# Optimization experiments

Hardware: AMD Instinct MI355X
Metric: run time of the kernel (lower is better)

Reference implementation:

```python
import jax, jax.numpy as jnp
import numpy as np

OBS, PRED = 8, 12
EIN, EHID, NOISE = 64, 256, 64
GEMB = 64
DHID = EHID + NOISE  # 320
G, NPER = 8, 192
B = G * NPER


def leaky(x):
    return jnp.where(x > 0, x, 0.2 * x)


def lstm_cell(x, h, c, Wih, Whh, bih, bhh):
    gates = x @ Wih.T + bih + h @ Whh.T + bhh
    i, f, g, o = jnp.split(gates, 4, axis=-1)
    c = jax.nn.sigmoid(f) * c + jax.nn.sigmoid(i) * jnp.tanh(g)
    h = jax.nn.sigmoid(o) * jnp.tanh(c)
    return h, c


def kmeans(x, k, niter=10):
    # deterministic init: first k points (torch used randperm)
    c = x[:k]
    ar = jnp.arange(k)
    for _ in range(niter):
        d2 = ((x[:, None, :] - c[None, :, :]) ** 2).sum(-1)  # [N,k]
        a = jnp.argmin(d2, axis=1)
        onehot = (a[:, None] == ar[None, :]).astype(x.dtype)  # [N,k]
        cnt = onehot.sum(0)
        mean = (onehot.T @ x) / jnp.maximum(cnt, 1.0)[:, None]
        c = jnp.where((cnt == 0)[:, None], x[:k], mean)  # reseed dead clusters
    d2 = ((x[:, None, :] - c[None, :, :]) ** 2).sum(-1)
    return jnp.argmin(d2, axis=1)


def signed_graph(node, W_ne, b_ne, W_att, b_att):
    n, D = node.shape
    emb = node @ W_ne.T + b_ne  # [n,E]
    E = emb.shape[1]
    a_other, a_self = W_att[0, :E], W_att[0, E:]
    # e[i,j] = a_other.emb[j] + a_self.emb[i] + b  (cat([other, self]) order)
    e = (emb @ a_other)[None, :] + (emb @ a_self)[:, None] + b_att[0]
    edge = jax.nn.softmax(leaky(e), axis=0)
    edge = jnp.triu(edge, 0) + jnp.triu(edge, 1).T  # symmetrize from upper tri
    d = edge.sum(1)
    L = jnp.diag(d) - edge
    dinv = 1.0 / jnp.sqrt(d)
    L_sym = dinv[:, None] * L * dinv[None, :]
    lam, H = jnp.linalg.eigh(jax.lax.stop_gradient(L_sym))  # ascending eigvals
    H = H[:, :2]  # two smallest
    Hn = H / jnp.sqrt((H ** 2).sum(1, keepdims=True))
    labels = kmeans(Hn, int(np.ceil(n / 2)))
    same = labels[:, None] == labels[None, :]
    NEG = jnp.float32(-1e8)
    pos_alpha = jax.nn.softmax(leaky(edge * jnp.where(same, 1.0, NEG)), axis=0)
    neg_alpha = jax.nn.softmax(leaky(edge * jnp.where(same, NEG, 1.0)), axis=0)
    feat = jax.nn.relu(pos_alpha[..., None] * node[None, :, :]) + \
           jax.nn.relu(neg_alpha[..., None] * node[None, :, :])  # [n,n,D]
    return feat.sum(axis=1)


def setup_inputs():
    key = jax.random.key(0)
    ks = jax.random.split(key, 22)
    p = lambda k, s: jax.random.normal(k, s, jnp.float32) * 0.1
    starts = jnp.arange(G, dtype=jnp.int32) * NPER
    return {
        "input_traj": jax.random.normal(ks[0], (OBS + PRED, B, 2), jnp.float32),
        "enc_h0": jax.random.normal(ks[1], (B, EHID), jnp.float32),
        "enc_c0": jax.random.normal(ks[2], (B, EHID), jnp.float32),
        "noise_z": jax.random.normal(ks[3], (G, NOISE), jnp.float32),
        "W_emb": p(ks[4], (EIN, 2)), "b_emb": p(ks[5], (EIN,)),
        "Wih_e": p(ks[6], (4 * EHID, EIN)), "Whh_e": p(ks[7], (4 * EHID, EHID)),
        "bih_e": p(ks[8], (4 * EHID,)), "bhh_e": p(ks[9], (4 * EHID,)),
        "Wih_d": p(ks[10], (4 * DHID, EIN)), "Whh_d": p(ks[11], (4 * DHID, DHID)),
        "bih_d": p(ks[12], (4 * DHID,)), "bhh_d": p(ks[13], (4 * DHID,)),
        "W_out": p(ks[14], (2, DHID)), "b_out": p(ks[15], (2,)),
        "W_ne": p(ks[16], (GEMB, DHID)), "b_ne": p(ks[17], (GEMB,)),
        "W_att": p(ks[18], (1, 2 * GEMB)), "b_att": p(ks[19], (1,)),
        "seq_start_end": jnp.stack([starts, starts + NPER], axis=1),
    }


def reference(input_traj, enc_h0, enc_c0, noise_z, W_emb, b_emb,
              Wih_e, Whh_e, bih_e, bhh_e, Wih_d, Whh_d, bih_d, bhh_d,
              W_out, b_out, W_ne, b_ne, W_att, b_att, seq_start_end):
    # ---- encoder ----
    x = jax.nn.relu(input_traj @ W_emb.T + b_emb)  # [T,B,EIN]
    def step(carry, xt):
        h, c = carry
        h, c = lstm_cell(xt, h, c, Wih_e, Whh_e, bih_e, bhh_e)
        return (h, c), None
    (h_enc, _), _ = jax.lax.scan(step, (enc_h0, enc_c0), x[:OBS])
    # ---- add per-scene noise (equal-sized scenes) ----
    z = jnp.repeat(noise_z, NPER, axis=0)  # [B,NOISE]
    h = jnp.concatenate([h_enc, z], axis=1)  # [B,DHID]
    c = jnp.zeros_like(h)
    traj_out = input_traj[OBS - 1]  # [B,2]
    sg = jax.vmap(lambda nd: signed_graph(nd, W_ne, b_ne, W_att, b_att))
    preds = []
    for i in range(PRED):  # eval mode: no teacher forcing
        inp = jax.nn.relu(traj_out @ W_emb.T + b_emb)
        if i % 12 == 4:
            h = sg(h.reshape(G, NPER, DHID)).reshape(B, DHID)
        h, c = lstm_cell(inp, h, c, Wih_d, Whh_d, bih_d, bhh_d)
        traj_out = h @ W_out.T + b_out
        preds.append(traj_out)
    return jnp.stack(preds)  # [PRED,B,2]
```

## Files before the change

kernel.cpp:

```cpp
#include <hip/hip_runtime.h>
#include <hip/hip_bf16.h>

typedef __hip_bfloat16 bf16;

#define NN 192
#define NG 8
#define BB 1536
#define EHID 256
#define DH 320
#define PRED 12
#define STRD 196

#define WAVE_SYNC() do { asm volatile("" ::: "memory"); __builtin_amdgcn_wave_barrier(); } while (0)

__device__ __forceinline__ float waveSum(float v){
#pragma unroll
  for (int o = 32; o > 0; o >>= 1) v += __shfl_down(v, o);
  return v;
}
__device__ __forceinline__ double waveSumD(double v){
#pragma unroll
  for (int o = 32; o > 0; o >>= 1) v += __shfl_down(v, o);
  return v;
}
__device__ __forceinline__ float waveAllSum(float v){
#pragma unroll
  for (int o = 32; o > 0; o >>= 1) v += __shfl_xor(v, o);
  return v;
}
__device__ __forceinline__ double waveAllSumD(double v){
#pragma unroll
  for (int o = 32; o > 0; o >>= 1) v += __shfl_xor(v, o);
  return v;
}

__device__ __forceinline__ double blockSumD(double v, double* red){
  int lane = threadIdx.x & 63, wid = threadIdx.x >> 6, nw = (int)blockDim.x >> 6;
  double s = waveSumD(v);
  __syncthreads();
  if (lane == 0) red[wid] = s;
  __syncthreads();
  if (wid == 0){
    double t = (lane < nw) ? red[lane] : 0.0;
    t = waveSumD(t);
    if (lane == 0) red[0] = t;
  }
  __syncthreads();
  return red[0];
}


__global__ void k_zero_int(int* __restrict__ p, int n){
  int i = blockIdx.x*blockDim.x + threadIdx.x;
  if (i < n) p[i] = 0;
}
__global__ void k_zero_f(float* __restrict__ p, int n){
  int i = blockIdx.x*blockDim.x + threadIdx.x;
  if (i < n) p[i] = 0.f;
}

__global__ void k_probe(const unsigned short* __restrict__ src, int n, int* __restrict__ cnt){
  int tid = blockIdx.x*blockDim.x + threadIdx.x;
  int stride = gridDim.x*blockDim.x;
  int bad = 0;
  for (int j = tid; j < n; j += stride){
    float v = __uint_as_float(((unsigned int)src[j]) << 16);
    if (!(fabsf(v) < 100.f)) bad++;
  }
#pragma unroll
  for (int o = 32; o > 0; o >>= 1) bad += __shfl_down(bad, o);
  if ((threadIdx.x & 63) == 0 && bad > 0) atomicAdd(cnt, bad);
}
__global__ void k_flag(const int* __restrict__ cnt, int* __restrict__ flag){
  *flag = (*cnt > 4096) ? 1 : 0;
}

struct CvtArgs {
  const void* src[20];
  float*      dst[20];
  int         n[20];
};

__global__ void k_convert(CvtArgs a, const int* __restrict__ flag){
  int id = blockIdx.y;
  int n = a.n[id];
  float* d = a.dst[id];
  int t = blockIdx.x*blockDim.x + threadIdx.x;
  int stride = gridDim.x*blockDim.x;
  if (*flag == 0){
    const bf16* s = (const bf16*)a.src[id];
    for (int j = t; j < n; j += stride) d[j] = __bfloat162float(s[j]);
  } else {
    const float* s = (const float*)a.src[id];
    for (int j = t; j < n; j += stride) d[j] = s[j];
  }
}


__global__ void k_embed(const float* __restrict__ in, const float* __restrict__ W,
                        const float* __restrict__ b, float* __restrict__ out){
  int r = blockIdx.x, e = threadIdx.x;
  float x = in[r*2], y = in[r*2+1];
  float v = W[e*2]*x + W[e*2+1]*y + b[e];
  out[r*64+e] = v > 0.f ? v : 0.f;
}

__global__ void k_concat(const float* __restrict__ henc, const float* __restrict__ z,
                         float* __restrict__ h){
  int idx = blockIdx.x*blockDim.x + threadIdx.x;
  if (idx >= BB*DH) return;
  int b = idx / DH, j = idx - b*DH;
  h[idx] = (j < EHID) ? henc[b*EHID + j] : z[(b/NN)*64 + (j - EHID)];
}

__global__ void k_copy_f(const float* __restrict__ in, float* __restrict__ dst, int n){
  int i = blockIdx.x*blockDim.x + threadIdx.x;
  if (i < n) dst[i] = in[i];
}

__global__ __launch_bounds__(256) void k_gates(
    const float* __restrict__ A1, const float* __restrict__ W1, int K1,
    const float* __restrict__ A2, const float* __restrict__ W2, int K2,
    const float* __restrict__ b1, const float* __restrict__ b2,
    float* __restrict__ C, int N){
  __shared__ __align__(16) float As[32][68];
  __shared__ __align__(16) float Ws[32][68];
  int tid = threadIdx.x;
  int tx = tid & 15, ty = tid >> 4;
  int n0 = blockIdx.x * 64, m0 = blockIdx.y * 64;
  float acc[4][4] = {};
  for (int ph = 0; ph < 2; ++ph){
    const float* A = ph ? A2 : A1;
    const float* W = ph ? W2 : W1;
    int K = ph ? K2 : K1;
    for (int k0 = 0; k0 < K; k0 += 32){
      {
        int am = tid >> 2, ak = (tid & 3) * 8;
        const float* srcA = A + (size_t)(m0+am)*K + k0 + ak;
        float4 f0 = *(const float4*)(srcA);
        float4 f1 = *(const float4*)(srcA+4);
        As[ak+0][am]=f0.x; As[ak+1][am]=f0.y; As[ak+2][am]=f0.z; As[ak+3][am]=f0.w;
        As[ak+4][am]=f1.x; As[ak+5][am]=f1.y; As[ak+6][am]=f1.z; As[ak+7][am]=f1.w;
        const float* srcW = W + (size_t)(n0+am)*K + k0 + ak;
        float4 w0 = *(const float4*)(srcW);
        float4 w1 = *(const float4*)(srcW+4);
        Ws[ak+0][am]=w0.x; Ws[ak+1][am]=w0.y; Ws[ak+2][am]=w0.z; Ws[ak+3][am]=w0.w;
        Ws[ak+4][am]=w1.x; Ws[ak+5][am]=w1.y; Ws[ak+6][am]=w1.z; Ws[ak+7][am]=w1.w;
      }
      __syncthreads();
#pragma unroll
      for (int k = 0; k < 32; ++k){
        float4 a0 = *(const float4*)&As[k][ty*4];
        float4 b0 = *(const float4*)&Ws[k][tx*4];
        float av[4] = {a0.x, a0.y, a0.z, a0.w};
        float bv[4] = {b0.x, b0.y, b0.z, b0.w};
#pragma unroll
        for (int i = 0; i < 4; ++i)
#pragma unroll
          for (int j = 0; j < 4; ++j)
            acc[i][j] += av[i]*bv[j];
      }
      __syncthreads();
    }
  }
  float bs[4];
#pragma unroll
  for (int j = 0; j < 4; ++j){
    int col = n0 + tx*4 + j;
    bs[j] = b1[col] + b2[col];
  }
#pragma unroll
  for (int i = 0; i < 4; ++i){
    int row = m0 + ty*4 + i;
    float4 v;
    v.x = acc[i][0] + bs[0]; v.y = acc[i][1] + bs[1];
    v.z = acc[i][2] + bs[2]; v.w = acc[i][3] + bs[3];
    *(float4*)&C[(size_t)row*N + n0 + tx*4] = v;
  }
}

__global__ void k_lstm(const float* __restrict__ gates, float* __restrict__ c,
                       float* __restrict__ h, int H){
  int idx = blockIdx.x*blockDim.x + threadIdx.x;
  if (idx >= BB*H) return;
  int b = idx / H, j = idx - b*H;
  const float* g = gates + (size_t)b*4*H;
  float gi = g[j], gf = g[H+j], gg = g[2*H+j], go = g[3*H+j];
  float si = 1.f/(1.f+expf(-gi));
  float sf = 1.f/(1.f+expf(-gf));
  float so = 1.f/(1.f+expf(-go));
  float cc = sf*c[idx] + si*tanhf(gg);
  c[idx] = cc;
  h[idx] = so*tanhf(cc);
}

__global__ void k_outproj(const float* __restrict__ h, const float* __restrict__ W,
                          const float* __restrict__ bo, float* __restrict__ traj,
                          void* __restrict__ outbase, int step, const int* __restrict__ flag){
  int b = blockIdx.x, lane = threadIdx.x;
  const float* hb = h + (size_t)b*DH;
  float a0 = 0.f, a1 = 0.f;
  for (int k = lane; k < DH; k += 64){
    float hv = hb[k];
    a0 += hv*W[k];
    a1 += hv*W[DH+k];
  }
  a0 = waveSum(a0); a1 = waveSum(a1);
  if (lane == 0){
    a0 += bo[0]; a1 += bo[1];
    traj[b*2] = a0; traj[b*2+1] = a1;
    size_t idx = (size_t)step*BB*2 + (size_t)b*2;
    if (*flag == 0){
      bf16* o = (bf16*)outbase;
      o[idx] = __float2bfloat16(a0); o[idx+1] = __float2bfloat16(a1);
    } else {
      float* o = (float*)outbase;
      o[idx] = a0; o[idx+1] = a1;
    }
  }
}


__global__ void k_sg_emb(const float* __restrict__ h, const float* __restrict__ Wne,
                         const float* __restrict__ bne, const float* __restrict__ Watt,
                         double* __restrict__ sself, double* __restrict__ sother){
  int node = blockIdx.x, e = threadIdx.x;
  const float* hb = h + (size_t)node*DH;
  double acc = (double)bne[e];
  for (int k = 0; k < DH; ++k) acc += (double)hb[k]*(double)Wne[e*DH+k];
  double po = acc * (double)Watt[e];
  double ps = acc * (double)Watt[64+e];
  po = waveSumD(po); ps = waveSumD(ps);
  if (e == 0){ sother[node] = po; sself[node] = ps; }
}

__global__ void k_sg_edgecol(const double* __restrict__ sself, const double* __restrict__ sother,
                             const float* __restrict__ batt, double* __restrict__ edge){
  int g = blockIdx.x, j = threadIdx.x;
  const double* ss = sself + g*NN;
  double bb = (double)batt[0];
  double sj = sother[g*NN + j];
  double m = -1e300;
  for (int i = 0; i < NN; ++i){
    double e = ss[i] + sj + bb; e = e > 0.0 ? e : 0.2*e;
    m = fmax(m, e);
  }
  double sum = 0.0;
  for (int i = 0; i < NN; ++i){
    double e = ss[i] + sj + bb; e = e > 0.0 ? e : 0.2*e;
    sum += exp(e - m);
  }
  double* E = edge + (size_t)g*NN*NN;
  for (int i = 0; i < NN; ++i){
    double e = ss[i] + sj + bb; e = e > 0.0 ? e : 0.2*e;
    E[i*NN + j] = exp(e - m)/sum;
  }
}

__global__ void k_sg_sym(const double* __restrict__ edge, double* __restrict__ esym){
  int idx = blockIdx.x*blockDim.x + threadIdx.x;
  if (idx >= NG*NN*NN) return;
  int g = idx / (NN*NN), r = idx - g*NN*NN;
  int i = r / NN, j = r - i*NN;
  const double* E = edge + (size_t)g*NN*NN;
  esym[idx] = (i <= j) ? E[i*NN + j] : E[j*NN + i];
}

__global__ void k_sg_dsum(const double* __restrict__ esym, double* __restrict__ darr){
  int i = blockIdx.x*blockDim.x + threadIdx.x;
  if (i >= NG*NN) return;
  int g = i / NN, li = i - g*NN;
  const double* E = esym + (size_t)g*NN*NN + (size_t)li*NN;
  double s = 0.0;
  for (int j = 0; j < NN; ++j) s += E[j];
  darr[i] = fmax(s, 1e-300);
}

__global__ void k_sg_lsym(const double* __restrict__ esym, const double* __restrict__ darr,
                          float* __restrict__ Afull){
  int idx = blockIdx.x*blockDim.x + threadIdx.x;
  if (idx >= NG*NN*NN) return;
  int g = idx / (NN*NN), r = idx - g*NN*NN;
  int i = r / NN, j = r - i*NN;
  double w = esym[idx];
  double lij = (i == j) ? (darr[g*NN+i] - w) : (-w);
  Afull[(size_t)g*NN*STRD + i*STRD + j] =
      (float)(lij / (sqrt(darr[g*NN+i])*sqrt(darr[g*NN+j])));
}

__global__ __launch_bounds__(256) void k_sg_eigen(const float* __restrict__ Afull,
                                                   const double* __restrict__ darr,
                                                   double* __restrict__ v1out){
  extern __shared__ unsigned char ldsraw[];
  float*  A     = (float*)ldsraw;
  double* dd    = (double*)(ldsraw + 150528);
  double* ee    = dd + NN;
  double* yv    = ee + NN;
  double* lu_d  = yv + NN;
  double* lu_du = lu_d + NN;
  double* lu_du2= lu_du + NN;
  double* redA  = lu_du2 + NN;
  double* redB  = redA + 16;
  float*  vv    = (float*)(redB + 16);
  float*  pp    = vv + NN;
  float*  uu    = pp + NN;
  int*    lu_piv= (int*)uu;
  double* lu_dl = (double*)vv;

  int g = blockIdx.x, tid = threadIdx.x;
  int lane = tid & 63, wid = tid >> 6;

  const float* src = Afull + (size_t)g*NN*STRD;
  for (int t = tid*4; t < NN*STRD; t += 1024) *(float4*)&A[t] = *(const float4*)&src[t];
  __syncthreads();

  for (int k = 0; k < NN-65; ++k){
    int m = NN-1-k;
    int i = k+1+tid;
    float x = 0.f;
    if (tid < m){
      x = A[i*STRD + k];
      vv[i] = x;
    }
    float part = (tid > 0 && tid < m) ? x*x : 0.f;
    part = waveSum(part);
    if (lane == 0) redA[wid] = (double)part;
    __syncthreads();
    double sigma = redA[0] + redA[1] + redA[2] + redA[3];
    double alpha = (double)vv[k+1];
    double beta, tau, scale;
    if (sigma <= 1e-30){ tau = 0.0; beta = alpha; scale = 0.0; }
    else {
      beta = -copysign(sqrt(alpha*alpha + sigma), alpha);
      tau = (beta - alpha)/beta;
      scale = 1.0/(alpha - beta);
    }
    float tau_f = (float)tau, scale_f = (float)scale;
    if (tid == 0){
      dd[k] = (double)A[k*STRD + k];
      ee[k] = beta;
      A[k*STRD + k] = tau_f;
    }
    if (tau != 0.0){
      float p = 0.f, u_i = 0.f;
      if (tid < m){
        const float* Ai = A + (size_t)i*STRD;
        if (tid >= 1) A[i*STRD + k] = x*scale_f;
        u_i = (tid == 0) ? 1.f : x*scale_f;
        float acc = 0.f;
        int c = k+2, c0 = (c + 3) & ~3;
        for (; c < c0; ++c) acc += Ai[c]*vv[c];
        for (; c < NN; c += 4){
          float4 a4 = *(const float4*)&Ai[c];
          float4 v4 = *(const float4*)&vv[c];
          acc += a4.x*v4.x + a4.y*v4.y + a4.z*v4.z + a4.w*v4.w;
        }
        float s = Ai[k+1] + scale_f*acc;
        p = tau_f*s;
        pp[i] = p;
      }
      float vp = u_i*p;
      vp = waveSum(vp);
      if (lane == 0) redB[wid] = (double)vp;
      __syncthreads();
      double vtp = redB[0] + redB[1] + redB[2] + redB[3];
      float Kc_f = (float)(0.5*tau*vtp);
      if (tid < m){
        float* Ai = A + (size_t)i*STRD;
        float w_i = p - Kc_f*u_i;
        {
          float wj = pp[k+1] - Kc_f;
          Ai[k+1] -= u_i*wj + w_i;
        }
        int c = k+2, c0 = (c + 3) & ~3;
        for (; c < c0; ++c){
          float uj = vv[c]*scale_f;
          float wj = pp[c] - Kc_f*uj;
          Ai[c] -= u_i*wj + w_i*uj;
        }
        for (; c < NN; c += 4){
          float4 v4 = *(const float4*)&vv[c];
          float4 p4 = *(const float4*)&pp[c];
          float4 a4 = *(const float4*)&Ai[c];
          float u0 = v4.x*scale_f, u1 = v4.y*scale_f, u2 = v4.z*scale_f, u3 = v4.w*scale_f;
          a4.x -= u_i*(p4.x - Kc_f*u0) + w_i*u0;
          a4.y -= u_i*(p4.y - Kc_f*u1) + w_i*u1;
          a4.z -= u_i*(p4.z - Kc_f*u2) + w_i*u2;
          a4.w -= u_i*(p4.w - Kc_f*u3) + w_i*u3;
          *(float4*)&Ai[c] = a4;
        }
      }
      __syncthreads();
    } else {
      __syncthreads();
    }
  }

  if (wid != 0) return;

  {
    float* uu_s = uu;
    float* ww_s = uu + 96;
    for (int k = NN-65; k < NN-2; ++k){
      int m = NN-1-k;
      int i = k+1+lane;
      bool act = lane < m;
      float x = act ? A[i*STRD + k] : 0.f;
      float part = (lane > 0) ? x*x : 0.f;
      float sig_f = waveAllSum(part);
      float alpha_f = __shfl(x, 0);
      double sigma = (double)sig_f;
      double alpha = (double)alpha_f;
      double beta, tau, scale;
      if (sigma <= 1e-30){ tau = 0.0; beta = alpha; scale = 0.0; }
      else {
        beta = -copysign(sqrt(alpha*alpha + sigma), alpha);
        tau = (beta - alpha)/beta;
        scale = 1.0/(alpha - beta);
      }
      float tau_f = (float)tau, scale_f = (float)scale;
      if (lane == 0){
        dd[k] = (double)A[k*STRD + k];
        ee[k] = beta;
        A[k*STRD + k] = tau_f;
      }
      if (tau == 0.0) continue;
      float u = (lane == 0) ? 1.f : x*scale_f;
      int base4 = (k+1) & ~3;
      int ph = (k+1) - base4;
      uu_s[lane + ph] = u;
      if (lane >= 1 && act) A[i*STRD + k] = u;
      WAVE_SYNC();
      int ic = act ? i : (k+1);
      const float* Ai = A + (size_t)ic*STRD;
      float acc = 0.f;
      {
        int c = k+1, c0 = (c + 3) & ~3;
        for (; c < c0; ++c) acc += Ai[c]*uu_s[c-base4];
        for (; c < NN; c += 4){
          float4 a4 = *(const float4*)&Ai[c];
          float4 u4 = *(const float4*)&uu_s[c-base4];
          acc += a4.x*u4.x + a4.y*u4.y + a4.z*u4.z + a4.w*u4.w;
        }
      }
      float p = tau_f*acc;
      float vtp = waveAllSum(u*p);
      float Kc_f = (float)(0.5*tau*(double)vtp);
      float w = p - Kc_f*u;
      ww_s[lane + ph] = w;
      WAVE_SYNC();
      if (act){
        float* Aw = A + (size_t)i*STRD;
        int c = k+1, c0 = (c + 3) & ~3;
        for (; c < c0; ++c){
          float uj = uu_s[c-base4], wj = ww_s[c-base4];
          Aw[c] -= u*wj + w*uj;
        }
        for (; c < NN; c += 4){
          float4 u4 = *(const float4*)&uu_s[c-base4];
          float4 w4 = *(const float4*)&ww_s[c-base4];
          float4 a4 = *(const float4*)&Aw[c];
          a4.x -= u*w4.x + w*u4.x;
          a4.y -= u*w4.y + w*u4.y;
          a4.z -= u*w4.z + w*u4.z;
          a4.w -= u*w4.w + w*u4.w;
          *(float4*)&Aw[c] = a4;
        }
      }
      WAVE_SYNC();
    }
  }

  if (lane == 0){
    dd[NN-2] = (double)A[(NN-2)*STRD + (NN-2)];
    ee[NN-2] = (double)A[(NN-1)*STRD + (NN-2)];
    dd[NN-1] = (double)A[(NN-1)*STRD + (NN-1)];
  }
  WAVE_SYNC();

  {
    double mn = 1e300, mx = -1e300;
    for (int i = lane; i < NN; i += 64){
      double r = (i > 0 ? fabs(ee[i-1]) : 0.0) + (i < NN-1 ? fabs(ee[i]) : 0.0);
      mn = fmin(mn, dd[i]-r); mx = fmax(mx, dd[i]+r);
    }
#pragma unroll
    for (int o = 32; o > 0; o >>= 1){
      mn = fmin(mn, __shfl_down(mn, o));
      mx = fmax(mx, __shfl_down(mx, o));
    }
    mn = __shfl(mn, 0); mx = __shfl(mx, 0);
    double lo = mn - 1e-8 - 1e-9*fabs(mn);
    double hi = mx + 1e-8 + 1e-9*fabs(mx);
    for (int it = 0; it < 10; ++it){
      double lam = lo + (hi-lo)*((double)(lane+1)/65.0);
      int cnt = 0;
      double q = dd[0] - lam;
      if (q < 0.0) cnt++;
      for (int i2 = 1; i2 < NN; ++i2){
        double den = q;
        if (fabs(den) < 1e-280) den = (den < 0.0) ? -1e-280 : 1e-280;
        q = dd[i2] - lam - ee[i2-1]*ee[i2-1]/den;
        if (q < 0.0) cnt++;
      }
      unsigned long long bal = __ballot(cnt >= 2);
      if (bal == 0ull){
        lo = lo + (hi-lo)*(64.0/65.0);
      } else {
        int j0 = __ffsll(bal) - 1;
        double nl = lo + (hi-lo)*((double)j0/65.0);
        double nh = lo + (hi-lo)*((double)(j0+1)/65.0);
        lo = nl; hi = nh;
      }
    }
    double lam1 = 0.5*(lo+hi);

    if (lane == 0){
      for (int i = 0; i < NN; ++i) lu_d[i] = dd[i] - lam1;
      for (int i = 0; i < NN-1; ++i){ lu_dl[i] = ee[i]; lu_du[i] = ee[i]; }
      for (int i = 0; i < NN-2; ++i) lu_du2[i] = 0.0;
      for (int i = 0; i < NN-1; ++i){
        if (fabs(lu_d[i]) >= fabs(lu_dl[i])){
          double di = lu_d[i];
          if (fabs(di) < 1e-30){ di = (di < 0.0) ? -1e-30 : 1e-30; lu_d[i] = di; }
          double fact = lu_dl[i]/di;
          lu_dl[i] = fact;
          lu_d[i+1] -= fact*lu_du[i];
          lu_piv[i] = 0;
        } else {
          double fact = lu_d[i]/lu_dl[i];
          lu_d[i] = lu_dl[i];
          double tmp = lu_d[i+1];
          lu_d[i+1] = lu_du[i] - fact*tmp;
          if (i < NN-2){ lu_du2[i] = lu_du[i+1]; lu_du[i+1] = -fact*lu_du[i+1]; }
          lu_du[i] = tmp;
          lu_dl[i] = fact;
          lu_piv[i] = 1;
        }
      }
      if (fabs(lu_d[NN-1]) < 1e-30)
        lu_d[NN-1] = (lu_d[NN-1] < 0.0) ? -1e-30 : 1e-30;
      for (int i = 0; i < NN; ++i) yv[i] = 1.0 + 0.001*(double)((i*37)%29);
      for (int round = 0; round < 2; ++round){
        for (int i = 0; i < NN-1; ++i){
          if (lu_piv[i] == 0){
            yv[i+1] -= lu_dl[i]*yv[i];
          } else {
            double t = yv[i]; yv[i] = yv[i+1]; yv[i+1] = t - lu_dl[i]*yv[i];
          }
        }
        double mx1 = 0.0;
        for (int i = 0; i < NN; ++i) mx1 = fmax(mx1, fabs(yv[i]));
        double inv1 = (mx1 > 0.0 && isfinite(mx1)) ? 1.0/mx1 : 1.0;
        for (int i = 0; i < NN; ++i) yv[i] *= inv1;
        yv[NN-1] = yv[NN-1]/lu_d[NN-1];
        yv[NN-2] = (yv[NN-2] - lu_du[NN-2]*yv[NN-1])/lu_d[NN-2];
        for (int i = NN-3; i >= 0; --i)
          yv[i] = (yv[i] - lu_du[i]*yv[i+1] - lu_du2[i]*yv[i+2])/lu_d[i];
        double mxv = 0.0;
        for (int i = 0; i < NN; ++i) mxv = fmax(mxv, fabs(yv[i]));
        double inv = (mxv > 0.0 && isfinite(mxv)) ? 1.0/mxv : 1.0;
        for (int i = 0; i < NN; ++i){
          double val = yv[i]*inv;
          if (!isfinite(val)) val = 0.0;
          yv[i] = val;
        }
      }
    }
  }
  WAVE_SYNC();

  {
    int r0 = lane, r1 = lane+64, r2 = lane+128;
    double y0 = yv[r0], y1 = yv[r1], y2 = yv[r2];
    for (int k = NN-3; k >= 0; --k){
      double tau = (double)A[k*STRD + k];
      if (tau != 0.0){
        double u0 = (r0 > k) ? ((r0 == k+1) ? 1.0 : (double)A[r0*STRD + k]) : 0.0;
        double u1 = (r1 > k) ? ((r1 == k+1) ? 1.0 : (double)A[r1*STRD + k]) : 0.0;
        double u2 = (r2 > k) ? ((r2 == k+1) ? 1.0 : (double)A[r2*STRD + k]) : 0.0;
        double part = u0*y0 + u1*y1 + u2*y2;
        part = waveAllSumD(part);
        double s = tau*part;
        y0 -= s*u0; y1 -= s*u1; y2 -= s*u2;
      }
    }

    const double* dg = darr + (size_t)g*NN;
    double d0 = dg[r0], d1 = dg[r1], d2 = dg[r2];
    double sd0 = sqrt(d0), sd1 = sqrt(d1), sd2 = sqrt(d2);
    double pd  = waveAllSumD(sd0*y0 + sd1*y1 + sd2*y2);
    double pn2 = waveAllSumD(d0 + d1 + d2);
    double coef = pd/fmax(pn2, 1e-300);
    y0 -= coef*sd0; y1 -= coef*sd1; y2 -= coef*sd2;
    double s2 = waveAllSumD(y0*y0 + y1*y1 + y2*y2);
    double nrm = sqrt(s2);
    double inv = (nrm > 0.0 && isfinite(nrm)) ? 1.0/nrm : 0.0;
    double o0 = y0*inv, o1 = y1*inv, o2 = y2*inv;
    if (!isfinite(o0)) o0 = 0.0;
    if (!isfinite(o1)) o1 = 0.0;
    if (!isfinite(o2)) o2 = 0.0;
    v1out[g*NN + r0] = o0;
    v1out[g*NN + r1] = o1;
    v1out[g*NN + r2] = o2;
  }
}

__global__ __launch_bounds__(256) void k_sg_kmeans(const double* __restrict__ darr,
                                                   const double* __restrict__ v1,
                                                   int* __restrict__ labels){
  __shared__ double px[NN], py[NN], cx[96], cy[96];
  __shared__ int lab[NN];
  __shared__ double red[16];
  int g = blockIdx.x, tid = threadIdx.x;
  double part = 0.0;
  for (int i = tid; i < NN; i += 256) part += darr[g*NN + i];
  double sumd = blockSumD(part, red);
  double invn = 1.0/sqrt(fmax(sumd, 1e-300));
  for (int i = tid; i < NN; i += 256){
    double h0 = sqrt(darr[g*NN + i])*invn;
    double h1 = v1[g*NN + i];
    double rn = sqrt(h0*h0 + h1*h1);
    double ax = h0/rn, ay = h1/rn;
    if (!isfinite(ax)) ax = 0.0;
    if (!isfinite(ay)) ay = 0.0;
    px[i] = ax; py[i] = ay;
  }
  __syncthreads();
  if (tid < 96){ cx[tid] = px[tid]; cy[tid] = py[tid]; }
  __syncthreads();
  for (int it = 0; it <= 10; ++it){
    if (tid < NN){
      double bx = px[tid], by = py[tid];
      double best = 1e300; int bi = 0;
      for (int a = 0; a < 96; ++a){
        double dx = bx - cx[a], dy = by - cy[a];
        double d2 = dx*dx + dy*dy;
        if (d2 < best){ best = d2; bi = a; }
      }
      lab[tid] = bi;
    }
    __syncthreads();
    if (it == 10) break;
    if (tid < 96){
      int c = 0; double sx = 0.0, sy = 0.0;
      for (int i = 0; i < NN; ++i){
        if (lab[i] == tid){ c++; sx += px[i]; sy += py[i]; }
      }
      if (c > 0){ cx[tid] = sx/(double)c; cy[tid] = sy/(double)c; }
      else      { cx[tid] = px[tid];      cy[tid] = py[tid]; }
    }
    __syncthreads();
  }
  if (tid < NN) labels[g*NN + tid] = lab[tid];
}

__global__ void k_sg_alpha(const double* __restrict__ esym, const int* __restrict__ labels,
                           float* __restrict__ S){
  __shared__ int lbs[NN];
  int g = blockIdx.x, j = threadIdx.x;
  if (j < NN) lbs[j] = labels[g*NN + j];
  __syncthreads();
  const double* E = esym + (size_t)g*NN*NN;
  const double NEG = -100000000.0;
  int lj = lbs[j];
  double mp = -1e300, mn = -1e300;
  for (int i = 0; i < NN; ++i){
    double w = E[i*NN + j];
    bool sm = (lbs[i] == lj);
    double vp = sm ? w : w*NEG; vp = vp > 0.0 ? vp : 0.2*vp;
    double vn = sm ? w*NEG : w; vn = vn > 0.0 ? vn : 0.2*vn;
    mp = fmax(mp, vp); mn = fmax(mn, vn);
  }
  double sp = 0.0, sn = 0.0;
  for (int i = 0; i < NN; ++i){
    double w = E[i*NN + j];
    bool sm = (lbs[i] == lj);
    double vp = sm ? w : w*NEG; vp = vp > 0.0 ? vp : 0.2*vp;
    double vn = sm ? w*NEG : w; vn = vn > 0.0 ? vn : 0.2*vn;
    sp += exp(vp - mp); sn += exp(vn - mn);
  }
  float* So = S + (size_t)g*NN*NN;
  for (int i = 0; i < NN; ++i){
    double w = E[i*NN + j];
    bool sm = (lbs[i] == lj);
    double vp = sm ? w : w*NEG; vp = vp > 0.0 ? vp : 0.2*vp;
    double vn = sm ? w*NEG : w; vn = vn > 0.0 ? vn : 0.2*vn;
    So[i*NN + j] = (float)(exp(vp - mp)/sp + exp(vn - mn)/sn);
  }
}

__global__ __launch_bounds__(320) void k_sg_feat(const float* __restrict__ S,
                                                 const float* __restrict__ hin,
                                                 float* __restrict__ hout){
  int r = blockIdx.x;
  int g = r / NN, li = r - g*NN;
  int dh = threadIdx.x;
  const float* Srow = S + (size_t)g*NN*NN + (size_t)li*NN;
  const float* hb = hin + (size_t)g*NN*DH;
  float acc = 0.f;
  for (int j = 0; j < NN; ++j){
    float w = Srow[j];
    float x = hb[(size_t)j*DH + dh];
    acc += w*(x > 0.f ? x : 0.f);
  }
  hout[(size_t)r*DH + dh] = acc;
}


extern "C" void kernel_launch(void* const* d_in, const int* in_sizes, int n_in,
                              void* d_out, int out_size, void* d_ws, size_t ws_size,
                              hipStream_t stream){
  (void)n_in; (void)out_size; (void)ws_size;

  float* ws = (float*)d_ws;
  float* inp   = ws;
  float* gates = ws + 98304;
  float* hA    = ws + 2064384;
  float* hB    = ws + 2555904;
  float* cD    = ws + 3047424;
  float* traj  = ws + 3538944;
  double* sself_d  = (double*)(ws + 3542016);
  double* sother_d = (double*)(ws + 3545088);
  double* darr_d   = (double*)(ws + 3548160);
  double* v1_d     = (double*)(ws + 3551232);
  int*    labels   = (int*)(ws + 3554304);
  double* edge_d = (double*)gates;
  double* esym_d = (double*)(gates + 589824);
  float*  Afull  = gates + 1179648;
  float*  Smat   = gates;
  float* a_traj = ws + 3555840;
  float* a_z    = ws + 3617280;
  float* a_Wemb = ws + 3617792;
  float* a_bemb = ws + 3617920;
  float* a_Wihe = ws + 3617984;
  float* a_Whhe = ws + 3683520;
  float* a_bihe = ws + 3945664;
  float* a_bhhe = ws + 3946688;
  float* a_Wihd = ws + 3947712;
  float* a_Whhd = ws + 4029632;
  float* a_bihd = ws + 4439232;
  float* a_bhhd = ws + 4440512;
  float* a_Wout = ws + 4441792;
  float* a_bout = ws + 4442432;
  float* a_Wne  = ws + 4442496;
  float* a_bne  = ws + 4462976;
  float* a_Watt = ws + 4463040;
  float* a_batt = ws + 4463168;
  int* cnt  = (int*)(ws + 4463232);
  int* flag = (int*)(ws + 4463233);

  const int EIG_LDS = 162304;
  hipFuncSetAttribute((const void*)k_sg_eigen,
                      hipFuncAttributeMaxDynamicSharedMemorySize, EIG_LDS);

  k_zero_int<<<1, 64, 0, stream>>>(cnt, 2);
  k_probe<<<256, 256, 0, stream>>>((const unsigned short*)d_in[1], in_sizes[1], cnt);
  k_flag<<<1, 1, 0, stream>>>(cnt, flag);

  CvtArgs ca;
  float* dsts[20] = { a_traj, hB, cD, a_z, a_Wemb, a_bemb, a_Wihe, a_Whhe, a_bihe,
                      a_bhhe, a_Wihd, a_Whhd, a_bihd, a_bhhd, a_Wout, a_bout,
                      a_Wne, a_bne, a_Watt, a_batt };
  for (int i = 0; i < 20; ++i){
    ca.src[i] = d_in[i];
    ca.dst[i] = dsts[i];
    ca.n[i]   = in_sizes[i];
  }
  k_convert<<<dim3(512, 20), 256, 0, stream>>>(ca, flag);

  for (int t = 0; t < 8; ++t){
    k_embed<<<BB, 64, 0, stream>>>(a_traj + (size_t)t*BB*2, a_Wemb, a_bemb, inp);
    k_gates<<<dim3(1024/64, BB/64), 256, 0, stream>>>(inp, a_Wihe, 64, hB, a_Whhe, EHID,
                                                      a_bihe, a_bhhe, gates, 1024);
    k_lstm<<<(BB*EHID+255)/256, 256, 0, stream>>>(gates, cD, hB, EHID);
  }

  k_concat<<<(BB*DH+255)/256, 256, 0, stream>>>(hB, a_z, hA);
  k_zero_f<<<(BB*DH+255)/256, 256, 0, stream>>>(cD, BB*DH);
  k_copy_f<<<(BB*2+255)/256, 256, 0, stream>>>(a_traj + (size_t)7*BB*2, traj, BB*2);

  float* hcur = hA;
  float* hoth = hB;
  for (int i = 0; i < PRED; ++i){
    k_embed<<<BB, 64, 0, stream>>>(traj, a_Wemb, a_bemb, inp);
    if (i == 4){
      k_sg_emb<<<BB, 64, 0, stream>>>(hcur, a_Wne, a_bne, a_Watt, sself_d, sother_d);
      k_sg_edgecol<<<NG, NN, 0, stream>>>(sself_d, sother_d, a_batt, edge_d);
      k_sg_sym<<<(NG*NN*NN+255)/256, 256, 0, stream>>>(edge_d, esym_d);
      k_sg_dsum<<<(NG*NN+255)/256, 256, 0, stream>>>(esym_d, darr_d);
      k_sg_lsym<<<(NG*NN*NN+255)/256, 256, 0, stream>>>(esym_d, darr_d, Afull);
      k_sg_eigen<<<NG, 256, EIG_LDS, stream>>>(Afull, darr_d, v1_d);
      k_sg_kmeans<<<NG, 256, 0, stream>>>(darr_d, v1_d, labels);
      k_sg_alpha<<<NG, NN, 0, stream>>>(esym_d, labels, Smat);
      k_sg_feat<<<BB, DH, 0, stream>>>(Smat, hcur, hoth);
      float* tmp = hcur; hcur = hoth; hoth = tmp;
    }
    k_gates<<<dim3((4*DH)/64, BB/64), 256, 0, stream>>>(inp, a_Wihd, 64, hcur, a_Whhd, DH,
                                                        a_bihd, a_bhhd, gates, 4*DH);
    k_lstm<<<(BB*DH+255)/256, 256, 0, stream>>>(gates, cD, hcur, DH);
    k_outproj<<<BB, 64, 0, stream>>>(hcur, a_Wout, a_bout, traj, d_out, i, flag);
  }
}
```

Before: 2.598 ms.

## Swizzle LDS matrix layout in Householder tridiagonalization to avoid bank conflicts

```diff
diff --git a/kernel.cpp b/kernel.cpp
--- a/kernel.cpp
+++ b/kernel.cpp
@@ -9,7 +9,14 @@
 #define EHID 256
 #define DH 320
 #define PRED 12
-#define STRD 196
+#define STRD 192
+#define ATILE (NN*STRD)
+
+__device__ __forceinline__ int aoffc(int r, int c){
+  int c4 = c >> 2;
+  int s = (c4 & ~7) | ((c4 + 3*r) & 7);
+  return r*STRD + (s << 2) + (c & 3);
+}
 
 #define WAVE_SYNC() do { asm volatile("" ::: "memory"); __builtin_amdgcn_wave_barrier(); } while (0)
 
@@ -284,7 +291,7 @@
   int i = r / NN, j = r - i*NN;
   double w = esym[idx];
   double lij = (i == j) ? (darr[g*NN+i] - w) : (-w);
-  Afull[(size_t)g*NN*STRD + i*STRD + j] =
+  Afull[(size_t)g*ATILE + aoffc(i, j)] =
       (float)(lij / (sqrt(darr[g*NN+i])*sqrt(darr[g*NN+j])));
 }
 
@@ -293,7 +300,7 @@
                                                    double* __restrict__ v1out){
   extern __shared__ unsigned char ldsraw[];
   float*  A     = (float*)ldsraw;
-  double* dd    = (double*)(ldsraw + 150528);
+  double* dd    = (double*)(ldsraw + 147456);
   double* ee    = dd + NN;
   double* yv    = ee + NN;
   double* lu_d  = yv + NN;
@@ -301,33 +308,31 @@
   double* lu_du2= lu_du + NN;
   double* redA  = lu_du2 + NN;
   double* redB  = redA + 16;
-  float*  vv    = (float*)(redB + 16);
-  float*  pp    = vv + NN;
-  float*  uu    = pp + NN;
-  int*    lu_piv= (int*)uu;
-  double* lu_dl = (double*)vv;
+  double* salpha= redB + 16;
+  float*  uu    = (float*)(ldsraw + 156944);
+  float*  ww    = uu + NN;
+  int*    lu_piv= (int*)(ww + NN);
+  double* lu_dl = (double*)uu;
 
   int g = blockIdx.x, tid = threadIdx.x;
   int lane = tid & 63, wid = tid >> 6;
 
-  const float* src = Afull + (size_t)g*NN*STRD;
-  for (int t = tid*4; t < NN*STRD; t += 1024) *(float4*)&A[t] = *(const float4*)&src[t];
+  const float* src = Afull + (size_t)g*ATILE;
+  for (int t = tid*4; t < ATILE; t += 1024) *(float4*)&A[t] = *(const float4*)&src[t];
   __syncthreads();
 
   for (int k = 0; k < NN-65; ++k){
     int m = NN-1-k;
     int i = k+1+tid;
     float x = 0.f;
-    if (tid < m){
-      x = A[i*STRD + k];
-      vv[i] = x;
-    }
+    if (tid < m) x = A[aoffc(i, k)];
+    if (tid == 0) *salpha = (double)x;
     float part = (tid > 0 && tid < m) ? x*x : 0.f;
     part = waveSum(part);
     if (lane == 0) redA[wid] = (double)part;
     __syncthreads();
     double sigma = redA[0] + redA[1] + redA[2] + redA[3];
-    double alpha = (double)vv[k+1];
+    double alpha = *salpha;
     double beta, tau, scale;
     if (sigma <= 1e-30){ tau = 0.0; beta = alpha; scale = 0.0; }
     else {
@@ -337,27 +342,45 @@
     }
     float tau_f = (float)tau, scale_f = (float)scale;
     if (tid == 0){
-      dd[k] = (double)A[k*STRD + k];
+      dd[k] = (double)A[aoffc(k, k)];
       ee[k] = beta;
-      A[k*STRD + k] = tau_f;
+      A[aoffc(k, k)] = tau_f;
     }
     if (tau != 0.0){
-      float p = 0.f, u_i = 0.f;
+      float u_i = 0.f;
       if (tid < m){
-        const float* Ai = A + (size_t)i*STRD;
-        if (tid >= 1) A[i*STRD + k] = x*scale_f;
         u_i = (tid == 0) ? 1.f : x*scale_f;
-        float acc = 0.f;
-        int c = k+2, c0 = (c + 3) & ~3;
-        for (; c < c0; ++c) acc += Ai[c]*vv[c];
-        for (; c < NN; c += 4){
-          float4 a4 = *(const float4*)&Ai[c];
-          float4 v4 = *(const float4*)&vv[c];
-          acc += a4.x*v4.x + a4.y*v4.y + a4.z*v4.z + a4.w*v4.w;
+        uu[i] = u_i;
+        if (tid >= 1) A[aoffc(i, k)] = u_i;
+      }
+      __syncthreads();
+      float p = 0.f;
+      if (tid < m){
+        const int rb = i*STRD;
+        const int rk3 = (3*i) & 7;
+        int off[8];
+#pragma unroll
+        for (int j = 0; j < 8; ++j) off[j] = ((j + rk3) & 7) << 2;
+        float s0=0.f, s1=0.f, s2=0.f, s3=0.f, accs=0.f;
+        int c = k+1;
+        int cA = (c+3)&~3, cB = (c+31)&~31;
+        for (; c < cA; ++c) accs += A[aoffc(i, c)]*uu[c];
+        for (; c < cB; c += 4){
+          int c4 = c>>2; int s = (c4&~7)|((c4+rk3)&7);
+          float4 a4 = *(const float4*)&A[rb + (s<<2)];
+          float4 u4 = *(const float4*)&uu[c];
+          s0 += a4.x*u4.x; s1 += a4.y*u4.y; s2 += a4.z*u4.z; s3 += a4.w*u4.w;
         }
-        float s = Ai[k+1] + scale_f*acc;
-        p = tau_f*s;
-        pp[i] = p;
+        for (; c < NN; c += 32){
+          const int cb = rb + c;
+#pragma unroll
+          for (int j = 0; j < 8; ++j){
+            float4 a4 = *(const float4*)&A[cb + off[j]];
+            float4 u4 = *(const float4*)&uu[c + 4*j];
+            s0 += a4.x*u4.x; s1 += a4.y*u4.y; s2 += a4.z*u4.z; s3 += a4.w*u4.w;
+          }
+        }
+        p = tau_f * (((s0+s1)+(s2+s3)) + accs);
       }
       float vp = u_i*p;
       vp = waveSum(vp);
@@ -365,29 +388,47 @@
       __syncthreads();
       double vtp = redB[0] + redB[1] + redB[2] + redB[3];
       float Kc_f = (float)(0.5*tau*vtp);
+      float w_i = 0.f;
       if (tid < m){
-        float* Ai = A + (size_t)i*STRD;
-        float w_i = p - Kc_f*u_i;
-        {
-          float wj = pp[k+1] - Kc_f;
-          Ai[k+1] -= u_i*wj + w_i;
+        w_i = p - Kc_f*u_i;
+        ww[i] = w_i;
+      }
+      __syncthreads();
+      if (tid < m){
+        const int rb = i*STRD;
+        const int rk3 = (3*i) & 7;
+        int off[8];
+#pragma unroll
+        for (int j = 0; j < 8; ++j) off[j] = ((j + rk3) & 7) << 2;
+        int c = k+1;
+        int cA = (c+3)&~3, cB = (c+31)&~31;
+        for (; c < cA; ++c) A[aoffc(i, c)] -= u_i*ww[c] + w_i*uu[c];
+        for (; c < cB; c += 4){
+          int c4 = c>>2; int s = (c4&~7)|((c4+rk3)&7);
+          float* ap = &A[rb + (s<<2)];
+          float4 a4 = *(const float4*)ap;
+          float4 u4 = *(const float4*)&uu[c];
+          float4 w4 = *(const float4*)&ww[c];
+          a4.x -= u_i*w4.x + w_i*u4.x;
+          a4.y -= u_i*w4.y + w_i*u4.y;
+          a4.z -= u_i*w4.z + w_i*u4.z;
+          a4.w -= u_i*w4.w + w_i*u4.w;
+          *(float4*)ap = a4;
         }
-        int c = k+2, c0 = (c + 3) & ~3;
-        for (; c < c0; ++c){
-          float uj = vv[c]*scale_f;
-          float wj = pp[c] - Kc_f*uj;
-          Ai[c] -= u_i*wj + w_i*uj;
-        }
-        for (; c < NN; c += 4){
-          float4 v4 = *(const float4*)&vv[c];
-          float4 p4 = *(const float4*)&pp[c];
-          float4 a4 = *(const float4*)&Ai[c];
-          float u0 = v4.x*scale_f, u1 = v4.y*scale_f, u2 = v4.z*scale_f, u3 = v4.w*scale_f;
-          a4.x -= u_i*(p4.x - Kc_f*u0) + w_i*u0;
-          a4.y -= u_i*(p4.y - Kc_f*u1) + w_i*u1;
-          a4.z -= u_i*(p4.z - Kc_f*u2) + w_i*u2;
-          a4.w -= u_i*(p4.w - Kc_f*u3) + w_i*u3;
-          *(float4*)&Ai[c] = a4;
+        for (; c < NN; c += 32){
+          const int cb = rb + c;
+#pragma unroll
+          for (int j = 0; j < 8; ++j){
+            float* ap = &A[cb + off[j]];
+            float4 a4 = *(const float4*)ap;
+            float4 u4 = *(const float4*)&uu[c + 4*j];
+            float4 w4 = *(const float4*)&ww[c + 4*j];
+            a4.x -= u_i*w4.x + w_i*u4.x;
+            a4.y -= u_i*w4.y + w_i*u4.y;
+            a4.z -= u_i*w4.z + w_i*u4.z;
+            a4.w -= u_i*w4.w + w_i*u4.w;
+            *(float4*)ap = a4;
+          }
         }
       }
       __syncthreads();
@@ -398,83 +439,81 @@
 
   if (wid != 0) return;
 
-  {
-    float* uu_s = uu;
-    float* ww_s = uu + 96;
-    for (int k = NN-65; k < NN-2; ++k){
-      int m = NN-1-k;
-      int i = k+1+lane;
-      bool act = lane < m;
-      float x = act ? A[i*STRD + k] : 0.f;
-      float part = (lane > 0) ? x*x : 0.f;
-      float sig_f = waveAllSum(part);
-      float alpha_f = __shfl(x, 0);
-      double sigma = (double)sig_f;
-      double alpha = (double)alpha_f;
-      double beta, tau, scale;
-      if (sigma <= 1e-30){ tau = 0.0; beta = alpha; scale = 0.0; }
-      else {
-        beta = -copysign(sqrt(alpha*alpha + sigma), alpha);
-        tau = (beta - alpha)/beta;
-        scale = 1.0/(alpha - beta);
-      }
-      float tau_f = (float)tau, scale_f = (float)scale;
-      if (lane == 0){
-        dd[k] = (double)A[k*STRD + k];
-        ee[k] = beta;
-        A[k*STRD + k] = tau_f;
-      }
-      if (tau == 0.0) continue;
-      float u = (lane == 0) ? 1.f : x*scale_f;
-      int base4 = (k+1) & ~3;
-      int ph = (k+1) - base4;
-      uu_s[lane + ph] = u;
-      if (lane >= 1 && act) A[i*STRD + k] = u;
-      WAVE_SYNC();
-      int ic = act ? i : (k+1);
-      const float* Ai = A + (size_t)ic*STRD;
-      float acc = 0.f;
-      {
-        int c = k+1, c0 = (c + 3) & ~3;
-        for (; c < c0; ++c) acc += Ai[c]*uu_s[c-base4];
-        for (; c < NN; c += 4){
-          float4 a4 = *(const float4*)&Ai[c];
-          float4 u4 = *(const float4*)&uu_s[c-base4];
-          acc += a4.x*u4.x + a4.y*u4.y + a4.z*u4.z + a4.w*u4.w;
-        }
-      }
-      float p = tau_f*acc;
-      float vtp = waveAllSum(u*p);
-      float Kc_f = (float)(0.5*tau*(double)vtp);
-      float w = p - Kc_f*u;
-      ww_s[lane + ph] = w;
-      WAVE_SYNC();
-      if (act){
-        float* Aw = A + (size_t)i*STRD;
-        int c = k+1, c0 = (c + 3) & ~3;
-        for (; c < c0; ++c){
-          float uj = uu_s[c-base4], wj = ww_s[c-base4];
-          Aw[c] -= u*wj + w*uj;
-        }
-        for (; c < NN; c += 4){
-          float4 u4 = *(const float4*)&uu_s[c-base4];
-          float4 w4 = *(const float4*)&ww_s[c-base4];
-          float4 a4 = *(const float4*)&Aw[c];
-          a4.x -= u*w4.x + w*u4.x;
-          a4.y -= u*w4.y + w*u4.y;
-          a4.z -= u*w4.z + w*u4.z;
-          a4.w -= u*w4.w + w*u4.w;
-          *(float4*)&Aw[c] = a4;
-        }
-      }
-      WAVE_SYNC();
-    }
+  for (int k = NN-65; k < NN-2; ++k){
+    int m = NN-1-k;
+    int i = k+1+lane;
+    bool act = lane < m;
+    float x = act ? A[aoffc(i, k)] : 0.f;
+    float part = (lane > 0) ? x*x : 0.f;
+    float sig_f = waveAllSum(part);
+    float alpha_f = __shfl(x, 0);
+    double sigma = (double)sig_f;
+    double alpha = (double)alpha_f;
+    double beta, tau, scale;
+    if (sigma <= 1e-30){ tau = 0.0; beta = alpha; scale = 0.0; }
+    else {
+      beta = -copysign(sqrt(alpha*alpha + sigma), alpha);
+      tau = (beta - alpha)/beta;
+      scale = 1.0/(alpha - beta);
+    }
+    float tau_f = (float)tau, scale_f = (float)scale;
+    if (lane == 0){
+      dd[k] = (double)A[aoffc(k, k)];
+      ee[k] = beta;
+      A[aoffc(k, k)] = tau_f;
+    }
+    if (tau == 0.0) continue;
+    float u = (lane == 0) ? 1.f : x*scale_f;
+    int base4 = (k+1) & ~3;
+    int ph = (k+1) - base4;
+    uu[lane + ph] = u;
+    if (lane >= 1 && act) A[aoffc(i, k)] = u;
+    WAVE_SYNC();
+    int ic = act ? i : (k+1);
+    const int rb = ic*STRD;
+    const int rk3 = (3*ic) & 7;
+    float s0=0.f, s1=0.f, s2=0.f, s3=0.f, accs=0.f;
+    {
+      int c = k+1;
+      int cA = (c+3)&~3; if (cA > NN) cA = NN;
+      for (; c < cA; ++c) accs += A[aoffc(ic, c)]*uu[c-base4];
+      for (; c < NN; c += 4){
+        int c4 = c>>2; int s = (c4&~7)|((c4+rk3)&7);
+        float4 a4 = *(const float4*)&A[rb + (s<<2)];
+        float4 u4 = *(const float4*)&uu[c-base4];
+        s0 += a4.x*u4.x; s1 += a4.y*u4.y; s2 += a4.z*u4.z; s3 += a4.w*u4.w;
+      }
+    }
+    float p = tau_f*(((s0+s1)+(s2+s3)) + accs);
+    float vtp = waveAllSum(u*p);
+    float Kc_f = (float)(0.5*tau*(double)vtp);
+    float w = p - Kc_f*u;
+    ww[lane + ph] = w;
+    WAVE_SYNC();
+    if (act){
+      int c = k+1;
+      int cA = (c+3)&~3; if (cA > NN) cA = NN;
+      for (; c < cA; ++c) A[aoffc(i, c)] -= u*ww[c-base4] + w*uu[c-base4];
+      for (; c < NN; c += 4){
+        int c4 = c>>2; int s = (c4&~7)|((c4+rk3)&7);
+        float* ap = &A[rb + (s<<2)];
+        float4 a4 = *(const float4*)ap;
+        float4 u4 = *(const float4*)&uu[c-base4];
+        float4 w4 = *(const float4*)&ww[c-base4];
+        a4.x -= u*w4.x + w*u4.x;
+        a4.y -= u*w4.y + w*u4.y;
+        a4.z -= u*w4.z + w*u4.z;
+        a4.w -= u*w4.w + w*u4.w;
+        *(float4*)ap = a4;
+      }
+    }
+    WAVE_SYNC();
   }
 
   if (lane == 0){
-    dd[NN-2] = (double)A[(NN-2)*STRD + (NN-2)];
-    ee[NN-2] = (double)A[(NN-1)*STRD + (NN-2)];
-    dd[NN-1] = (double)A[(NN-1)*STRD + (NN-1)];
+    dd[NN-2] = (double)A[aoffc(NN-2, NN-2)];
+    ee[NN-2] = (double)A[aoffc(NN-1, NN-2)];
+    dd[NN-1] = (double)A[aoffc(NN-1, NN-1)];
   }
   WAVE_SYNC();
 
@@ -574,11 +613,11 @@
     int r0 = lane, r1 = lane+64, r2 = lane+128;
     double y0 = yv[r0], y1 = yv[r1], y2 = yv[r2];
     for (int k = NN-3; k >= 0; --k){
-      double tau = (double)A[k*STRD + k];
+      double tau = (double)A[aoffc(k, k)];
       if (tau != 0.0){
-        double u0 = (r0 > k) ? ((r0 == k+1) ? 1.0 : (double)A[r0*STRD + k]) : 0.0;
-        double u1 = (r1 > k) ? ((r1 == k+1) ? 1.0 : (double)A[r1*STRD + k]) : 0.0;
-        double u2 = (r2 > k) ? ((r2 == k+1) ? 1.0 : (double)A[r2*STRD + k]) : 0.0;
+        double u0 = (r0 > k) ? ((r0 == k+1) ? 1.0 : (double)A[aoffc(r0, k)]) : 0.0;
+        double u1 = (r1 > k) ? ((r1 == k+1) ? 1.0 : (double)A[aoffc(r1, k)]) : 0.0;
+        double u2 = (r2 > k) ? ((r2 == k+1) ? 1.0 : (double)A[aoffc(r2, k)]) : 0.0;
         double part = u0*y0 + u1*y1 + u2*y2;
         part = waveAllSumD(part);
         double s = tau*part;
@@ -750,7 +789,7 @@
   int* cnt  = (int*)(ws + 4463232);
   int* flag = (int*)(ws + 4463233);
 
-  const int EIG_LDS = 162304;
+  const int EIG_LDS = 159248;
   hipFuncSetAttribute((const void*)k_sg_eigen,
                       hipFuncAttributeMaxDynamicSharedMemorySize, EIG_LDS);
 
```

Measured after the change: 2.315 ms. 1.12x faster.
